# Kernel tuning notes

Hardware: AMD Instinct MI355X
Metric: run time of the kernel (lower is better)

Reference implementation:

```python
import jax, jax.numpy as jnp
import numpy as np


def conv2d(x, w, b, pad=0, groups=1):
    y = jax.lax.conv_general_dilated(
        x, w, (1, 1), [(pad, pad), (pad, pad)],
        dimension_numbers=('NCHW', 'OIHW', 'NCHW'), feature_group_count=groups)
    return y + b[None, :, None, None]


def layernorm(x, w, b, eps=1e-5):
    # per-pixel LayerNorm over channel dim (matches to_3d -> nn.LayerNorm(dim) -> to_4d)
    mu = x.mean(1, keepdims=True)
    var = ((x - mu) ** 2).mean(1, keepdims=True)
    return (x - mu) * jax.lax.rsqrt(var + eps) * w[None, :, None, None] + b[None, :, None, None]


def setup_inputs():
    key = jax.random.key(0)
    ks = jax.random.split(key, 16)
    B, C, H, W = 1, 64, 64, 64
    heads, dh = 8, 8
    inner = heads * dh          # 64
    hid_lc = 32                 # max(16, inner // 2)
    hid_f = 4 * C               # 256, ffn_expansion_factor = 4
    def s(k, shape, fan):
        return (jax.random.normal(k, shape, jnp.float32) / np.float32(np.sqrt(fan)))
    return {
        'x': jax.random.normal(ks[0], (B, C, H, W), jnp.float32),
        'luma': jax.random.uniform(ks[1], (B, 1, H, W), jnp.float32),
        'ln1_w': jnp.ones((C,), jnp.float32), 'ln1_b': jnp.zeros((C,), jnp.float32),
        'qkv_w': s(ks[2], (3 * inner, C, 1, 1), C), 'qkv_b': jnp.zeros((3 * inner,), jnp.float32),
        'proj_w': s(ks[3], (C, inner, 1, 1), inner), 'proj_b': jnp.zeros((C,), jnp.float32),
        'lc1_w': s(ks[4], (hid_lc, 1, 3, 3), 9), 'lc1_b': jnp.zeros((hid_lc,), jnp.float32),
        'lc2_w': s(ks[5], (hid_lc, hid_lc, 3, 3), 9 * hid_lc), 'lc2_b': jnp.zeros((hid_lc,), jnp.float32),
        'gam_w': s(ks[6], (inner, hid_lc, 1, 1), hid_lc), 'gam_b': jnp.zeros((inner,), jnp.float32),
        'bet_w': s(ks[7], (inner, hid_lc, 1, 1), hid_lc), 'bet_b': jnp.zeros((inner,), jnp.float32),
        'alpha': jnp.float32(0.1),
        'ln2_w': jnp.ones((C,), jnp.float32), 'ln2_b': jnp.zeros((C,), jnp.float32),
        'ffn1_w': s(ks[8], (hid_f, C, 1, 1), C), 'ffn1_b': jnp.zeros((hid_f,), jnp.float32),
        'dw_w': s(ks[9], (hid_f, 1, 3, 3), 9), 'dw_b': jnp.zeros((hid_f,), jnp.float32),
        'ffn2_w': s(ks[10], (C, hid_f, 1, 1), hid_f), 'ffn2_b': jnp.zeros((C,), jnp.float32),
    }


def reference(x, luma, ln1_w, ln1_b, qkv_w, qkv_b, proj_w, proj_b,
              lc1_w, lc1_b, lc2_w, lc2_b, gam_w, gam_b, bet_w, bet_b, alpha,
              ln2_w, ln2_b, ffn1_w, ffn1_b, dw_w, dw_b, ffn2_w, ffn2_b):
    B, C, H, W = x.shape
    heads = 8
    N = H * W
    # --- attention branch ---
    xn = layernorm(x, ln1_w, ln1_b)
    qkv = conv2d(xn, qkv_w, qkv_b)             # [B, 3*inner, H, W]
    inner = qkv.shape[1] // 3
    dh = inner // heads

    def to_bhnd(t):  # b (h d) x y -> b h (x y) d
        return t.reshape(B, heads, dh, N).transpose(0, 1, 3, 2)

    q, k, v = [to_bhnd(t) for t in jnp.split(qkv, 3, axis=1)]
    # luma conditioning
    h1 = jax.nn.relu(conv2d(luma, lc1_w, lc1_b, pad=1))
    h1 = jax.nn.relu(conv2d(h1, lc2_w, lc2_b, pad=1))
    g = to_bhnd(conv2d(h1, gam_w, gam_b))
    bt = to_bhnd(conv2d(h1, bet_w, bet_b))
    q = g * q + bt
    k = g * k + bt
    v = g * v + bt
    # additive luma bias on q (avg_pool2d 3x3, count_include_pad=True -> fixed /9)
    invL = 1.0 - luma
    invL = jax.lax.reduce_window(invL, 0.0, jax.lax.add, (1, 1, 3, 3), (1, 1, 1, 1),
                                 [(0, 0), (0, 0), (1, 1), (1, 1)]) / 9.0
    invL = invL.reshape(B, N)
    invL = invL - invL.mean(-1, keepdims=True)
    q = q + alpha * invL[:, None, :, None]
    scale = dh ** -0.5
    attn = jax.nn.softmax(jnp.einsum('bhid,bhjd->bhij', q, k) * scale, axis=-1)
    out = jnp.einsum('bhij,bhjd->bhid', attn, v)
    out = out.transpose(0, 1, 3, 2).reshape(B, inner, H, W)
    x = x + conv2d(out, proj_w, proj_b)
    # --- ConvFFN branch ---
    y = layernorm(x, ln2_w, ln2_b)
    y = conv2d(y, ffn1_w, ffn1_b)
    y = conv2d(y, dw_w, dw_b, pad=1, groups=y.shape[1])
    y = jax.nn.gelu(y, approximate=False)
    y = conv2d(y, ffn2_w, ffn2_b)
    return x + y
```

## Files before the change

kernel.cpp:

```cpp
#include <hip/hip_runtime.h>
#include <math.h>

#define NPIX 4096
#define IMG 64

typedef __attribute__((ext_vector_type(8))) short bf16x8;
typedef __attribute__((ext_vector_type(4))) float floatx4;
typedef __attribute__((ext_vector_type(4))) unsigned int uintx4;

__device__ __forceinline__ unsigned int split_pack(float x) {
  unsigned int u = __float_as_uint(x);
  unsigned int hif = u & 0xffff0000u;
  float lof = x - __uint_as_float(hif);
  return (u >> 16) | (__float_as_uint(lof) & 0xffff0000u);
}

__device__ __forceinline__ unsigned int hi_pair(float a, float b) {
  return (__float_as_uint(a) >> 16) | (__float_as_uint(b) & 0xffff0000u);
}

__global__ __launch_bounds__(256) void lc1_kernel(
    const float* __restrict__ luma, const float* __restrict__ w1,
    const float* __restrict__ b1, float* __restrict__ h1,
    float* __restrict__ pooled, float* __restrict__ bsums,
    unsigned short* __restrict__ cbuf) {
  __shared__ float red[256];
  int tile = blockIdx.x, ocg = blockIdx.y;
  int tid = threadIdx.x;
  if (tile == 0 && ocg == 0 && tid < 16) cbuf[tid] = (tid < 8) ? 0x3F80 : 0;
  int p = tile * 256 + tid;
  int py = p >> 6, px = p & 63;
  float v[9];
#pragma unroll
  for (int dy = 0; dy < 3; dy++)
#pragma unroll
    for (int dx = 0; dx < 3; dx++) {
      int y = py + dy - 1, x = px + dx - 1;
      v[dy * 3 + dx] =
          (y >= 0 && y < IMG && x >= 0 && x < IMG) ? luma[y * IMG + x] : 0.f;
    }
#pragma unroll
  for (int o = 0; o < 4; o++) {
    int oc = ocg * 4 + o;
    float s = b1[oc];
#pragma unroll
    for (int t = 0; t < 9; t++) s = fmaf(w1[oc * 9 + t], v[t], s);
    h1[oc * NPIX + p] = fmaxf(s, 0.f);
  }
  if (ocg == 0) {
    float sv = 0.f;
#pragma unroll
    for (int t = 0; t < 9; t++) sv += v[t];
    float cy = 3.f - (py == 0 ? 1.f : 0.f) - (py == 63 ? 1.f : 0.f);
    float cx = 3.f - (px == 0 ? 1.f : 0.f) - (px == 63 ? 1.f : 0.f);
    float pv = (cy * cx - sv) * (1.f / 9.f);
    pooled[p] = pv;
    red[tid] = pv;
    __syncthreads();
    for (int st = 128; st > 0; st >>= 1) {
      if (tid < st) red[tid] += red[tid + st];
      __syncthreads();
    }
    if (tid == 0) bsums[tile] = red[0];
  }
}

__global__ __launch_bounds__(256) void lc2_kernel(
    const float* __restrict__ h1, const float* __restrict__ w2,
    const float* __restrict__ b2, const float* __restrict__ x,
    float* __restrict__ h2, float* __restrict__ mu1, float* __restrict__ rs1) {
  __shared__ float tin[32][324];
  __shared__ float swt[4][32][9];
  int tile = blockIdx.x, ocg = blockIdx.y;
  int ty0 = (tile >> 2) * 16, tx0 = (tile & 3) * 16;
  int tid = threadIdx.x;
  for (int idx = tid; idx < 32 * 324; idx += 256) {
    int ic = idx / 324, pos = idx - ic * 324;
    int py = pos / 18, px = pos - py * 18;
    int gy = ty0 + py - 1, gx = tx0 + px - 1;
    tin[ic][pos] = (gy >= 0 && gy < IMG && gx >= 0 && gx < IMG)
                       ? h1[ic * NPIX + gy * IMG + gx]
                       : 0.f;
  }
  for (int idx = tid; idx < 4 * 32 * 9; idx += 256) {
    int o = idx / 288, r = idx - o * 288;
    swt[o][r / 9][r % 9] = w2[(ocg * 4 + o) * 288 + r];
  }
  __syncthreads();
  int ly = tid >> 4, lx = tid & 15;
  int p = (ty0 + ly) * IMG + tx0 + lx;
  float acc[4];
#pragma unroll
  for (int o = 0; o < 4; o++) acc[o] = b2[ocg * 4 + o];
  for (int ic = 0; ic < 32; ic++) {
    float v[9];
#pragma unroll
    for (int dy = 0; dy < 3; dy++)
#pragma unroll
      for (int dx = 0; dx < 3; dx++)
        v[dy * 3 + dx] = tin[ic][(ly + dy) * 18 + lx + dx];
#pragma unroll
    for (int o = 0; o < 4; o++)
#pragma unroll
      for (int t = 0; t < 9; t++) acc[o] = fmaf(swt[o][ic][t], v[t], acc[o]);
  }
#pragma unroll
  for (int o = 0; o < 4; o++)
    h2[(ocg * 4 + o) * NPIX + p] = fmaxf(acc[o], 0.f);
  if (ocg == 0) {
    float s = 0.f, q = 0.f;
#pragma unroll 8
    for (int cc = 0; cc < 64; cc++) {
      float xv = x[cc * NPIX + p];
      s += xv;
      q = fmaf(xv, xv, q);
    }
    float mu = s * (1.f / 64.f);
    mu1[p] = mu;
    rs1[p] = rsqrtf(q * (1.f / 64.f) - mu * mu + 1e-5f);
  }
}

__global__ __launch_bounds__(256) void ln_qkv_kernel(
    const float* __restrict__ X, const float* __restrict__ mu1,
    const float* __restrict__ rs1, const float* __restrict__ lnw,
    const float* __restrict__ lnb, const float* __restrict__ W,
    const float* __restrict__ bias, const float* __restrict__ gamW,
    const float* __restrict__ gamB, const float* __restrict__ betW,
    const float* __restrict__ betB, const float* __restrict__ h2,
    const float* __restrict__ pooled, const float* __restrict__ bsums,
    const float* __restrict__ alpha, unsigned short* __restrict__ qhl,
    unsigned short* __restrict__ khl, unsigned short* __restrict__ vthx,
    unsigned short* __restrict__ vtlx) {
  const float QSCALE = 0.35355339059327376f * 1.4426950408889634f;
  __shared__ float xs[64][64];
  __shared__ float wsh[64][64];
  __shared__ float h2s[32][64];
  __shared__ float wgs[32][64];
  __shared__ float wbs[32][64];
  __shared__ float mu[64];
  __shared__ float rs[64];
  int n0 = blockIdx.x * 64, part = blockIdx.y, m0 = part * 64;
  int tid = threadIdx.x;
  int c = tid >> 2, pg = (tid & 3) * 16;
  if (tid < 64) {
    mu[tid] = mu1[n0 + tid];
    rs[tid] = rs1[n0 + tid];
  }
  {
    const float4* src = (const float4*)&X[c * NPIX + n0 + pg];
    float4* dst = (float4*)&xs[c][pg];
    dst[0] = src[0]; dst[1] = src[1]; dst[2] = src[2]; dst[3] = src[3];
  }
  {
    int m = tid >> 2, kg = (tid & 3) * 16;
    const float4* wr = (const float4*)&W[(m0 + m) * 64 + kg];
    float4 w0 = wr[0], w1 = wr[1], w2 = wr[2], w3 = wr[3];
    float wv[16] = {w0.x, w0.y, w0.z, w0.w, w1.x, w1.y, w1.z, w1.w,
                    w2.x, w2.y, w2.z, w2.w, w3.x, w3.y, w3.z, w3.w};
#pragma unroll
    for (int j = 0; j < 16; j++) wsh[kg + j][m] = wv[j];
  }
  {
    int i0 = tid * 2;
    int k = i0 >> 4, nf = (i0 & 15) * 4;
    *(float4*)&h2s[k][nf] = *(const float4*)&h2[k * NPIX + n0 + nf];
    int i1 = i0 + 1;
    int k1 = i1 >> 4, nf1 = (i1 & 15) * 4;
    *(float4*)&h2s[k1][nf1] = *(const float4*)&h2[k1 * NPIX + n0 + nf1];
  }
  {
    int m = tid >> 2, kg = (tid & 3) * 8;
    const float4* g0 = (const float4*)&gamW[m * 32 + kg];
    float4 a = g0[0], b4 = g0[1];
    float gv[8] = {a.x, a.y, a.z, a.w, b4.x, b4.y, b4.z, b4.w};
#pragma unroll
    for (int j = 0; j < 8; j++) wgs[kg + j][m] = gv[j];
    const float4* bb0 = (const float4*)&betW[m * 32 + kg];
    float4 c4 = bb0[0], d4 = bb0[1];
    float bv[8] = {c4.x, c4.y, c4.z, c4.w, d4.x, d4.y, d4.z, d4.w};
#pragma unroll
    for (int j = 0; j < 8; j++) wbs[kg + j][m] = bv[j];
  }
  __syncthreads();
  {
    float wc = lnw[c], bc = lnb[c];
#pragma unroll
    for (int j = 0; j < 16; j++) {
      int p = pg + j;
      xs[c][p] = (xs[c][p] - mu[p]) * rs[p] * wc + bc;
    }
  }
  __syncthreads();
  int tx = tid & 15, ty = tid >> 4;
  float ga[4][4] = {}, ba[4][4] = {};
#pragma unroll 8
  for (int kk = 0; kk < 32; kk++) {
    float4 wg4 = *(const float4*)&wgs[kk][ty * 4];
    float4 wb4 = *(const float4*)&wbs[kk][ty * 4];
    float4 h24 = *(const float4*)&h2s[kk][tx * 4];
    float gv[4] = {wg4.x, wg4.y, wg4.z, wg4.w};
    float bv[4] = {wb4.x, wb4.y, wb4.z, wb4.w};
    float hv[4] = {h24.x, h24.y, h24.z, h24.w};
#pragma unroll
    for (int im = 0; im < 4; im++)
#pragma unroll
      for (int in = 0; in < 4; in++) {
        ga[im][in] = fmaf(gv[im], hv[in], ga[im][in]);
        ba[im][in] = fmaf(bv[im], hv[in], ba[im][in]);
      }
  }
#pragma unroll
  for (int im = 0; im < 4; im++) {
    int cc = ty * 4 + im;
    float gb = gamB[cc], bb2 = betB[cc];
#pragma unroll
    for (int in = 0; in < 4; in++) {
      ga[im][in] += gb;
      ba[im][in] += bb2;
    }
  }
  float acc[4][4] = {};
#pragma unroll 8
  for (int kk = 0; kk < 64; kk++) {
    float4 a = *(const float4*)&wsh[kk][ty * 4];
    float4 b4 = *(const float4*)&xs[kk][tx * 4];
    float av[4] = {a.x, a.y, a.z, a.w};
    float bv[4] = {b4.x, b4.y, b4.z, b4.w};
#pragma unroll
    for (int im = 0; im < 4; im++)
#pragma unroll
      for (int in = 0; in < 4; in++)
        acc[im][in] = fmaf(av[im], bv[in], acc[im][in]);
  }
  float val[4][4];
#pragma unroll
  for (int im = 0; im < 4; im++) {
    int cc = ty * 4 + im;
    float bv = bias[m0 + cc];
#pragma unroll
    for (int in = 0; in < 4; in++)
      val[im][in] = fmaf(ga[im][in], acc[im][in] + bv, ba[im][in]);
  }
  if (part == 0) {
    float msum = 0.f;
#pragma unroll
    for (int t = 0; t < 16; t++) msum += bsums[t];
    float mean = msum * (1.f / 4096.f);
    float a0 = alpha[0];
    const float4 pv = *(const float4*)&pooled[n0 + tx * 4];
    float iv[4] = {a0 * (pv.x - mean), a0 * (pv.y - mean),
                   a0 * (pv.z - mean), a0 * (pv.w - mean)};
#pragma unroll
    for (int im = 0; im < 4; im++)
#pragma unroll
      for (int in = 0; in < 4; in++)
        val[im][in] = (val[im][in] + iv[in]) * QSCALE;
  }
  if (part < 2) {
    unsigned short* dst = (part == 0) ? qhl : khl;
    int h = ty >> 1, d0 = (ty & 1) * 4;
#pragma unroll
    for (int in = 0; in < 4; in++) {
      int n = n0 + tx * 4 + in;
      unsigned int pk[4];
#pragma unroll
      for (int im = 0; im < 4; im++) pk[im] = split_pack(val[im][in]);
      short4 hi, lo;
      hi.x = (short)(pk[0] & 0xffffu); hi.y = (short)(pk[1] & 0xffffu);
      hi.z = (short)(pk[2] & 0xffffu); hi.w = (short)(pk[3] & 0xffffu);
      lo.x = (short)(pk[0] >> 16); lo.y = (short)(pk[1] >> 16);
      lo.z = (short)(pk[2] >> 16); lo.w = (short)(pk[3] >> 16);
      unsigned short* base = dst + ((size_t)(h * NPIX + n) << 4) + d0;
      *(short4*)base = hi;
      *(short4*)(base + 8) = lo;
    }
  } else {
    int nq = n0 + tx * 4;
    int off0 = (nq >> 5) * 32 + ((nq >> 4) & 1) * 4 + ((nq >> 2) & 3) * 8;
#pragma unroll
    for (int im = 0; im < 4; im++) {
      int cc = ty * 4 + im;
      unsigned int pk[4];
#pragma unroll
      for (int in = 0; in < 4; in++) pk[in] = split_pack(val[im][in]);
      short4 hi, lo;
      hi.x = (short)(pk[0] & 0xffffu); hi.y = (short)(pk[1] & 0xffffu);
      hi.z = (short)(pk[2] & 0xffffu); hi.w = (short)(pk[3] & 0xffffu);
      lo.x = (short)(pk[0] >> 16); lo.y = (short)(pk[1] >> 16);
      lo.z = (short)(pk[2] >> 16); lo.w = (short)(pk[3] >> 16);
      *(short4*)(vthx + (size_t)cc * NPIX + off0) = hi;
      *(short4*)(vtlx + (size_t)cc * NPIX + off0) = lo;
    }
  }
}

__global__ __launch_bounds__(256, 6) void attn_kernel(
    const unsigned short* __restrict__ qhl,
    const unsigned short* __restrict__ khl,
    const unsigned short* __restrict__ vthx,
    const unsigned short* __restrict__ vtlx,
    const unsigned short* __restrict__ cbuf, float* __restrict__ pacc,
    float* __restrict__ pl) {
  int tid = threadIdx.x;
  int wave = tid >> 6, lane = tid & 63;
  int g = lane >> 4, c = lane & 15;
  int h = blockIdx.y, jp = blockIdx.z;
  int i0 = blockIdx.x * 128 + wave * 32;
  int jbase = jp * 512;
  const bf16x8 qB0 = *(const bf16x8*)(qhl + ((size_t)(h * NPIX + i0 + c) << 4) +
                                      ((g & 1) << 3));
  const bf16x8 qB1 = *(const bf16x8*)(
      qhl + ((size_t)(h * NPIX + i0 + 16 + c) << 4) + ((g & 1) << 3));
  const unsigned short* kp =
      khl + ((size_t)(h * NPIX + jbase + c) << 4) + ((g >> 1) << 3);
  const unsigned short* vhp;
  const unsigned short* vlp;
  int vstep;
  if (c < 8) {
    vhp = vthx + (size_t)(h * 8 + c) * NPIX + jbase + (g << 3);
    vlp = vtlx + (size_t)(h * 8 + c) * NPIX + jbase + (g << 3);
    vstep = 32;
  } else {
    vhp = (c == 8) ? cbuf : (cbuf + 8);
    vlp = cbuf + 8;
    vstep = 0;
  }
  floatx4 zero4 = {0.f, 0.f, 0.f, 0.f};
  floatx4 aH0 = zero4, aM0 = zero4, aH1 = zero4, aM1 = zero4;
#pragma unroll 2
  for (int jt = 0; jt < 16; ++jt) {
    bf16x8 ka0 = *(const bf16x8*)kp;
    bf16x8 ka1 = *(const bf16x8*)(kp + 256);
    bf16x8 avh = *(const bf16x8*)vhp;
    bf16x8 avl = *(const bf16x8*)vlp;
    kp += 512;
    vhp += vstep;
    vlp += vstep;
    floatx4 s00 =
        __builtin_amdgcn_mfma_f32_16x16x32_bf16(ka0, qB0, zero4, 0, 0, 0);
    floatx4 s01 =
        __builtin_amdgcn_mfma_f32_16x16x32_bf16(ka1, qB0, zero4, 0, 0, 0);
    floatx4 s10 =
        __builtin_amdgcn_mfma_f32_16x16x32_bf16(ka0, qB1, zero4, 0, 0, 0);
    floatx4 s11 =
        __builtin_amdgcn_mfma_f32_16x16x32_bf16(ka1, qB1, zero4, 0, 0, 0);
    {
      float p0 = __builtin_amdgcn_exp2f(fminf(s00[0], 80.f));
      float p1 = __builtin_amdgcn_exp2f(fminf(s00[1], 80.f));
      float p2 = __builtin_amdgcn_exp2f(fminf(s00[2], 80.f));
      float p3 = __builtin_amdgcn_exp2f(fminf(s00[3], 80.f));
      float p4 = __builtin_amdgcn_exp2f(fminf(s01[0], 80.f));
      float p5 = __builtin_amdgcn_exp2f(fminf(s01[1], 80.f));
      float p6 = __builtin_amdgcn_exp2f(fminf(s01[2], 80.f));
      float p7 = __builtin_amdgcn_exp2f(fminf(s01[3], 80.f));
      uintx4 bh;
      bh.x = hi_pair(p0, p1);
      bh.y = hi_pair(p2, p3);
      bh.z = hi_pair(p4, p5);
      bh.w = hi_pair(p6, p7);
      bf16x8 pbh = __builtin_bit_cast(bf16x8, bh);
      aH0 = __builtin_amdgcn_mfma_f32_16x16x32_bf16(avh, pbh, aH0, 0, 0, 0);
      aM0 = __builtin_amdgcn_mfma_f32_16x16x32_bf16(avl, pbh, aM0, 0, 0, 0);
    }
    {
      float p0 = __builtin_amdgcn_exp2f(fminf(s10[0], 80.f));
      float p1 = __builtin_amdgcn_exp2f(fminf(s10[1], 80.f));
      float p2 = __builtin_amdgcn_exp2f(fminf(s10[2], 80.f));
      float p3 = __builtin_amdgcn_exp2f(fminf(s10[3], 80.f));
      float p4 = __builtin_amdgcn_exp2f(fminf(s11[0], 80.f));
      float p5 = __builtin_amdgcn_exp2f(fminf(s11[1], 80.f));
      float p6 = __builtin_amdgcn_exp2f(fminf(s11[2], 80.f));
      float p7 = __builtin_amdgcn_exp2f(fminf(s11[3], 80.f));
      uintx4 bh;
      bh.x = hi_pair(p0, p1);
      bh.y = hi_pair(p2, p3);
      bh.z = hi_pair(p4, p5);
      bh.w = hi_pair(p6, p7);
      bf16x8 pbh = __builtin_bit_cast(bf16x8, bh);
      aH1 = __builtin_amdgcn_mfma_f32_16x16x32_bf16(avh, pbh, aH1, 0, 0, 0);
      aM1 = __builtin_amdgcn_mfma_f32_16x16x32_bf16(avl, pbh, aM1, 0, 0, 0);
    }
  }
  floatx4 o0 = aH0 + aM0;
  floatx4 o1 = aH1 + aM1;
  if (g < 2) {
    size_t b0 = (size_t)((jp * 8 + h) * NPIX + i0 + c);
    *(float4*)&pacc[b0 * 8 + g * 4] = make_float4(o0[0], o0[1], o0[2], o0[3]);
    size_t b1 = b0 + 16;
    *(float4*)&pacc[b1 * 8 + g * 4] = make_float4(o1[0], o1[1], o1[2], o1[3]);
  } else if (g == 2) {
    pl[(size_t)((jp * 8 + h) * NPIX + i0 + c)] = o0[0];
    pl[(size_t)((jp * 8 + h) * NPIX + i0 + 16 + c)] = o1[0];
  }
}

__global__ __launch_bounds__(256) void proj_ffn1_kernel(
    const float* __restrict__ pacc, const float* __restrict__ pl,
    const float* __restrict__ Wp, const float* __restrict__ bp,
    const float* __restrict__ x, const float* __restrict__ ln2w,
    const float* __restrict__ ln2b, const float* __restrict__ W1,
    const float* __restrict__ b1f, float* __restrict__ x1,
    float* __restrict__ f1) {
  __shared__ float at[64][33];
  __shared__ float wsh[64][64];
  __shared__ float xsl[64][33];
  __shared__ float ps[8][33];
  __shared__ float pq[8][33];
  __shared__ float mus[32];
  __shared__ float rss[32];
  int n0 = blockIdx.x * 32;
  int ch = blockIdx.y;
  int tid = threadIdx.x;
  {
    int mm = tid >> 2, kg = (tid & 3) * 16;
    const float4* wr = (const float4*)&Wp[mm * 64 + kg];
    float4 w0 = wr[0], w1 = wr[1], w2 = wr[2], w3 = wr[3];
    float wv[16] = {w0.x, w0.y, w0.z, w0.w, w1.x, w1.y, w1.z, w1.w,
                    w2.x, w2.y, w2.z, w2.w, w3.x, w3.y, w3.z, w3.w};
#pragma unroll
    for (int j = 0; j < 16; j++) wsh[kg + j][mm] = wv[j];
  }
  {
    int hh = tid >> 5, nn = tid & 31;
    int i = n0 + nn;
    float L = 0.f, o[8] = {};
#pragma unroll
    for (int p = 0; p < 8; p++) {
      size_t base = (size_t)((p * 8 + hh) * NPIX + i);
      L += pl[base];
      const float4 a0 = *(const float4*)&pacc[base * 8];
      const float4 a1 = *(const float4*)&pacc[base * 8 + 4];
      o[0] += a0.x; o[1] += a0.y; o[2] += a0.z; o[3] += a0.w;
      o[4] += a1.x; o[5] += a1.y; o[6] += a1.z; o[7] += a1.w;
    }
    float inv = 1.f / L;
#pragma unroll
    for (int d = 0; d < 8; d++) at[hh * 8 + d][nn] = o[d] * inv;
  }
  __syncthreads();
  int ty = tid >> 5, tx = tid & 31;
  float acc[8] = {};
#pragma unroll 8
  for (int k = 0; k < 64; k++) {
    float b = at[k][tx];
    float4 a0 = *(const float4*)&wsh[k][ty * 8];
    float4 a1 = *(const float4*)&wsh[k][ty * 8 + 4];
    acc[0] = fmaf(a0.x, b, acc[0]);
    acc[1] = fmaf(a0.y, b, acc[1]);
    acc[2] = fmaf(a0.z, b, acc[2]);
    acc[3] = fmaf(a0.w, b, acc[3]);
    acc[4] = fmaf(a1.x, b, acc[4]);
    acc[5] = fmaf(a1.y, b, acc[5]);
    acc[6] = fmaf(a1.z, b, acc[6]);
    acc[7] = fmaf(a1.w, b, acc[7]);
  }
  float v[8], sn = 0.f, qn = 0.f;
#pragma unroll
  for (int im = 0; im < 8; im++) {
    int row = ty * 8 + im;
    float vv = acc[im] + bp[row] + x[row * NPIX + n0 + tx];
    v[im] = vv;
    sn += vv;
    qn = fmaf(vv, vv, qn);
  }
  if (ch == 0) {
#pragma unroll
    for (int im = 0; im < 8; im++)
      x1[(ty * 8 + im) * NPIX + n0 + tx] = v[im];
  }
  ps[ty][tx] = sn;
  pq[ty][tx] = qn;
  __syncthreads();
  if (tid < 32) {
    float s = 0.f, q = 0.f;
#pragma unroll
    for (int t = 0; t < 8; t++) {
      s += ps[t][tid];
      q += pq[t][tid];
    }
    float mu = s * (1.f / 64.f);
    mus[tid] = mu;
    rss[tid] = rsqrtf(q * (1.f / 64.f) - mu * mu + 1e-5f);
  }
  __syncthreads();
  {
    float muv = mus[tx], rsv = rss[tx];
#pragma unroll
    for (int im = 0; im < 8; im++) {
      int row = ty * 8 + im;
      xsl[row][tx] = (v[im] - muv) * rsv * ln2w[row] + ln2b[row];
    }
  }
  {
    int mm = tid >> 2, kg = (tid & 3) * 16;
    const float4* wr = (const float4*)&W1[(ch * 64 + mm) * 64 + kg];
    float4 w0 = wr[0], w1 = wr[1], w2 = wr[2], w3 = wr[3];
    float wv[16] = {w0.x, w0.y, w0.z, w0.w, w1.x, w1.y, w1.z, w1.w,
                    w2.x, w2.y, w2.z, w2.w, w3.x, w3.y, w3.z, w3.w};
#pragma unroll
    for (int j = 0; j < 16; j++) wsh[kg + j][mm] = wv[j];
  }
  __syncthreads();
  float a2[8] = {};
#pragma unroll 8
  for (int k = 0; k < 64; k++) {
    float b = xsl[k][tx];
    float4 a0 = *(const float4*)&wsh[k][ty * 8];
    float4 a1 = *(const float4*)&wsh[k][ty * 8 + 4];
    a2[0] = fmaf(a0.x, b, a2[0]);
    a2[1] = fmaf(a0.y, b, a2[1]);
    a2[2] = fmaf(a0.z, b, a2[2]);
    a2[3] = fmaf(a0.w, b, a2[3]);
    a2[4] = fmaf(a1.x, b, a2[4]);
    a2[5] = fmaf(a1.y, b, a2[5]);
    a2[6] = fmaf(a1.z, b, a2[6]);
    a2[7] = fmaf(a1.w, b, a2[7]);
  }
#pragma unroll
  for (int im = 0; im < 8; im++) {
    int row = ch * 64 + ty * 8 + im;
    f1[row * NPIX + n0 + tx] = a2[im] + b1f[row];
  }
}

__global__ __launch_bounds__(256) void dw_gelu_kernel(
    const float* __restrict__ f1, const float* __restrict__ w,
    const float* __restrict__ b, float* __restrict__ f2) {
  int t = blockIdx.x * 256 + threadIdx.x;
  int c = t >> 10, pq = t & 1023;
  int py = pq >> 4, px0 = (pq & 15) << 2;
  const float* base = f1 + c * NPIX;
  float wv[9];
#pragma unroll
  for (int i = 0; i < 9; i++) wv[i] = w[c * 9 + i];
  float bc = b[c];
  float a[4] = {bc, bc, bc, bc};
#pragma unroll
  for (int dy = 0; dy < 3; dy++) {
    int y = py + dy - 1;
    if (y < 0 || y > 63) continue;
    const float* row = base + y * IMG + px0;
    float4 mid = *(const float4*)row;
    float left = (px0 > 0) ? row[-1] : 0.f;
    float right = (px0 < 60) ? row[4] : 0.f;
    float win[6] = {left, mid.x, mid.y, mid.z, mid.w, right};
#pragma unroll
    for (int o = 0; o < 4; o++)
#pragma unroll
      for (int dx = 0; dx < 3; dx++)
        a[o] = fmaf(wv[dy * 3 + dx], win[o + dx], a[o]);
  }
  float4 o4;
  float* op = &o4.x;
#pragma unroll
  for (int o = 0; o < 4; o++)
    op[o] = 0.5f * a[o] * (1.f + erff(a[o] * 0.70710678118654752f));
  *(float4*)&f2[c * NPIX + py * IMG + px0] = o4;
}

__global__ __launch_bounds__(256) void gemm16_kernel(
    const float* __restrict__ W, const float* __restrict__ X,
    const float* __restrict__ bias, const float* __restrict__ resid,
    float* __restrict__ C, int K) {
  __shared__ float xs[32][64];
  __shared__ float wsh[32][16];
  int n0 = blockIdx.x * 64, m0 = blockIdx.y * 16;
  int tid = threadIdx.x;
  int m = tid >> 4, ng = tid & 15;
  float acc[4] = {};
  for (int k0 = 0; k0 < K; k0 += 32) {
    {
      int i0 = tid * 2;
      int k = i0 >> 4, nf = (i0 & 15) * 4;
      *(float4*)&xs[k][nf] = *(const float4*)&X[(k0 + k) * NPIX + n0 + nf];
      int i1 = i0 + 1;
      int k1 = i1 >> 4, nf1 = (i1 & 15) * 4;
      *(float4*)&xs[k1][nf1] = *(const float4*)&X[(k0 + k1) * NPIX + n0 + nf1];
    }
#pragma unroll
    for (int e = tid; e < 512; e += 256) {
      int mm = e >> 5, kk = e & 31;
      wsh[kk][mm] = W[(m0 + mm) * K + k0 + kk];
    }
    __syncthreads();
#pragma unroll 8
    for (int kk = 0; kk < 32; kk++) {
      float a = wsh[kk][m];
      float4 b4 = *(const float4*)&xs[kk][ng * 4];
      acc[0] = fmaf(a, b4.x, acc[0]);
      acc[1] = fmaf(a, b4.y, acc[1]);
      acc[2] = fmaf(a, b4.z, acc[2]);
      acc[3] = fmaf(a, b4.w, acc[3]);
    }
    __syncthreads();
  }
  int row = m0 + m;
  float bv = bias[row];
  float4 o = make_float4(acc[0] + bv, acc[1] + bv, acc[2] + bv, acc[3] + bv);
  const float4 r4 = *(const float4*)&resid[row * NPIX + n0 + ng * 4];
  o.x += r4.x; o.y += r4.y; o.z += r4.z; o.w += r4.w;
  *(float4*)&C[row * NPIX + n0 + ng * 4] = o;
}

extern "C" void kernel_launch(void* const* d_in, const int* in_sizes, int n_in,
                              void* d_out, int out_size, void* d_ws,
                              size_t ws_size, hipStream_t stream) {
  const float* x      = (const float*)d_in[0];
  const float* luma   = (const float*)d_in[1];
  const float* ln1_w  = (const float*)d_in[2];
  const float* ln1_b  = (const float*)d_in[3];
  const float* qkv_w  = (const float*)d_in[4];
  const float* qkv_b  = (const float*)d_in[5];
  const float* proj_w = (const float*)d_in[6];
  const float* proj_b = (const float*)d_in[7];
  const float* lc1_w  = (const float*)d_in[8];
  const float* lc1_b  = (const float*)d_in[9];
  const float* lc2_w  = (const float*)d_in[10];
  const float* lc2_b  = (const float*)d_in[11];
  const float* gam_w  = (const float*)d_in[12];
  const float* gam_b  = (const float*)d_in[13];
  const float* bet_w  = (const float*)d_in[14];
  const float* bet_b  = (const float*)d_in[15];
  const float* alpha  = (const float*)d_in[16];
  const float* ln2_w  = (const float*)d_in[17];
  const float* ln2_b  = (const float*)d_in[18];
  const float* ffn1_w = (const float*)d_in[19];
  const float* ffn1_b = (const float*)d_in[20];
  const float* dw_w   = (const float*)d_in[21];
  const float* dw_b   = (const float*)d_in[22];
  const float* ffn2_w = (const float*)d_in[23];
  const float* ffn2_b = (const float*)d_in[24];
  float* out = (float*)d_out;

  float* w = (float*)d_ws;
  float* pooled = w + 0;
  float* bsums  = w + 4096;
  unsigned short* cbuf = (unsigned short*)(w + 4160);
  float* mu1 = w + 4224;
  float* rs1 = w + 8320;
  unsigned short* qhl  = (unsigned short*)(w + 12416);
  unsigned short* khl  = (unsigned short*)(w + 274560);
  unsigned short* vthx = (unsigned short*)(w + 536704);
  unsigned short* vtlx = (unsigned short*)(w + 667776);
  float* pacc = w + 798848;
  float* pl   = w + 2896000;
  float* x1   = w + 3158144;
  float* f1   = w + 3420288;
  float* f2   = w + 4468864;
  float* h2   = w + 5517440;
  float* h1   = w + 5648512;

  lc1_kernel<<<dim3(16, 8), 256, 0, stream>>>(luma, lc1_w, lc1_b, h1, pooled,
                                              bsums, cbuf);
  lc2_kernel<<<dim3(16, 8), 256, 0, stream>>>(h1, lc2_w, lc2_b, x, h2, mu1,
                                              rs1);
  ln_qkv_kernel<<<dim3(64, 3), 256, 0, stream>>>(
      x, mu1, rs1, ln1_w, ln1_b, qkv_w, qkv_b, gam_w, gam_b, bet_w, bet_b, h2,
      pooled, bsums, alpha, qhl, khl, vthx, vtlx);
  attn_kernel<<<dim3(32, 8, 8), 256, 0, stream>>>(qhl, khl, vthx, vtlx, cbuf,
                                                  pacc, pl);
  proj_ffn1_kernel<<<dim3(128, 4), 256, 0, stream>>>(
      pacc, pl, proj_w, proj_b, x, ln2_w, ln2_b, ffn1_w, ffn1_b, x1, f1);
  dw_gelu_kernel<<<1024, 256, 0, stream>>>(f1, dw_w, dw_b, f2);
  gemm16_kernel<<<dim3(64, 4), 256, 0, stream>>>(ffn2_w, f2, ffn2_b, x1, out,
                                                 256);
}
```

Before: 205.9 us.

## Halve attention key-split count and load full K in single-pass FFN2 kernel

The attention kernel now splits keys into 4 partitions of 1024 instead of 8 of 512. That halves the partial accumulator traffic and the reduction work in the proj kernel, but leaves fewer blocks in flight, so the occupancy hint drops from 6 to 4. The FFN2 GEMM is rewritten to stage all 256 K values of X and W in shared memory at once, using 32-column tiles and doubling the grid, which removes the per-chunk sync loop. This raises shared memory per block to about 48KB, which may limit occupancy.

```diff
diff --git a/kernel.cpp b/kernel.cpp
--- a/kernel.cpp
+++ b/kernel.cpp
@@ -295,7 +295,7 @@
   }
 }
 
-__global__ __launch_bounds__(256, 6) void attn_kernel(
+__global__ __launch_bounds__(256, 4) void attn_kernel(
     const unsigned short* __restrict__ qhl,
     const unsigned short* __restrict__ khl,
     const unsigned short* __restrict__ vthx,
@@ -307,7 +307,7 @@
   int g = lane >> 4, c = lane & 15;
   int h = blockIdx.y, jp = blockIdx.z;
   int i0 = blockIdx.x * 128 + wave * 32;
-  int jbase = jp * 512;
+  int jbase = jp * 1024;
   const bf16x8 qB0 = *(const bf16x8*)(qhl + ((size_t)(h * NPIX + i0 + c) << 4) +
                                       ((g & 1) << 3));
   const bf16x8 qB1 = *(const bf16x8*)(
@@ -329,7 +329,7 @@
   floatx4 zero4 = {0.f, 0.f, 0.f, 0.f};
   floatx4 aH0 = zero4, aM0 = zero4, aH1 = zero4, aM1 = zero4;
 #pragma unroll 2
-  for (int jt = 0; jt < 16; ++jt) {
+  for (int jt = 0; jt < 32; ++jt) {
     bf16x8 ka0 = *(const bf16x8*)kp;
     bf16x8 ka1 = *(const bf16x8*)(kp + 256);
     bf16x8 avh = *(const bf16x8*)vhp;
@@ -426,7 +426,7 @@
     int i = n0 + nn;
     float L = 0.f, o[8] = {};
 #pragma unroll
-    for (int p = 0; p < 8; p++) {
+    for (int p = 0; p < 4; p++) {
       size_t base = (size_t)((p * 8 + hh) * NPIX + i);
       L += pl[base];
       const float4 a0 = *(const float4*)&pacc[base * 8];
@@ -559,48 +559,39 @@
   *(float4*)&f2[c * NPIX + py * IMG + px0] = o4;
 }
 
-__global__ __launch_bounds__(256) void gemm16_kernel(
+__global__ __launch_bounds__(256) void ffn2_kernel(
     const float* __restrict__ W, const float* __restrict__ X,
     const float* __restrict__ bias, const float* __restrict__ resid,
-    float* __restrict__ C, int K) {
-  __shared__ float xs[32][64];
-  __shared__ float wsh[32][16];
-  int n0 = blockIdx.x * 64, m0 = blockIdx.y * 16;
+    float* __restrict__ C) {
+  __shared__ float xs[256][32];
+  __shared__ float wsh[256][16];
+  int n0 = blockIdx.x * 32, m0 = blockIdx.y * 16;
   int tid = threadIdx.x;
-  int m = tid >> 4, ng = tid & 15;
-  float acc[4] = {};
-  for (int k0 = 0; k0 < K; k0 += 32) {
-    {
-      int i0 = tid * 2;
-      int k = i0 >> 4, nf = (i0 & 15) * 4;
-      *(float4*)&xs[k][nf] = *(const float4*)&X[(k0 + k) * NPIX + n0 + nf];
-      int i1 = i0 + 1;
-      int k1 = i1 >> 4, nf1 = (i1 & 15) * 4;
-      *(float4*)&xs[k1][nf1] = *(const float4*)&X[(k0 + k1) * NPIX + n0 + nf1];
-    }
-#pragma unroll
-    for (int e = tid; e < 512; e += 256) {
-      int mm = e >> 5, kk = e & 31;
-      wsh[kk][mm] = W[(m0 + mm) * K + k0 + kk];
-    }
-    __syncthreads();
+#pragma unroll
+  for (int e = tid; e < 2048; e += 256) {
+    int k = e >> 3, nf = (e & 7) * 4;
+    *(float4*)&xs[k][nf] = *(const float4*)&X[k * NPIX + n0 + nf];
+  }
+#pragma unroll
+  for (int e = tid; e < 4096; e += 256) {
+    int mm = e >> 8, kk = e & 255;
+    wsh[kk][mm] = W[(m0 + mm) * 256 + kk];
+  }
+  __syncthreads();
+  int m = tid >> 4, np = (tid & 15) * 2;
+  float acc0 = 0.f, acc1 = 0.f;
 #pragma unroll 8
-    for (int kk = 0; kk < 32; kk++) {
-      float a = wsh[kk][m];
-      float4 b4 = *(const float4*)&xs[kk][ng * 4];
-      acc[0] = fmaf(a, b4.x, acc[0]);
-      acc[1] = fmaf(a, b4.y, acc[1]);
-      acc[2] = fmaf(a, b4.z, acc[2]);
-      acc[3] = fmaf(a, b4.w, acc[3]);
-    }
-    __syncthreads();
+  for (int kk = 0; kk < 256; kk++) {
+    float a = wsh[kk][m];
+    float2 b2 = *(const float2*)&xs[kk][np];
+    acc0 = fmaf(a, b2.x, acc0);
+    acc1 = fmaf(a, b2.y, acc1);
   }
   int row = m0 + m;
   float bv = bias[row];
-  float4 o = make_float4(acc[0] + bv, acc[1] + bv, acc[2] + bv, acc[3] + bv);
-  const float4 r4 = *(const float4*)&resid[row * NPIX + n0 + ng * 4];
-  o.x += r4.x; o.y += r4.y; o.z += r4.z; o.w += r4.w;
-  *(float4*)&C[row * NPIX + n0 + ng * 4] = o;
+  const float2 r2 = *(const float2*)&resid[row * NPIX + n0 + np];
+  float2 o = make_float2(acc0 + bv + r2.x, acc1 + bv + r2.y);
+  *(float2*)&C[row * NPIX + n0 + np] = o;
 }
 
 extern "C" void kernel_launch(void* const* d_in, const int* in_sizes, int n_in,
@@ -644,12 +635,12 @@
   unsigned short* vthx = (unsigned short*)(w + 536704);
   unsigned short* vtlx = (unsigned short*)(w + 667776);
   float* pacc = w + 798848;
-  float* pl   = w + 2896000;
-  float* x1   = w + 3158144;
-  float* f1   = w + 3420288;
-  float* f2   = w + 4468864;
-  float* h2   = w + 5517440;
-  float* h1   = w + 5648512;
+  float* pl   = w + 1847424;
+  float* x1   = w + 1978496;
+  float* f1   = w + 2240640;
+  float* f2   = w + 3289216;
+  float* h2   = w + 4337792;
+  float* h1   = w + 4468864;
 
   lc1_kernel<<<dim3(16, 8), 256, 0, stream>>>(luma, lc1_w, lc1_b, h1, pooled,
                                               bsums, cbuf);
@@ -658,11 +649,10 @@
   ln_qkv_kernel<<<dim3(64, 3), 256, 0, stream>>>(
       x, mu1, rs1, ln1_w, ln1_b, qkv_w, qkv_b, gam_w, gam_b, bet_w, bet_b, h2,
       pooled, bsums, alpha, qhl, khl, vthx, vtlx);
-  attn_kernel<<<dim3(32, 8, 8), 256, 0, stream>>>(qhl, khl, vthx, vtlx, cbuf,
+  attn_kernel<<<dim3(32, 8, 4), 256, 0, stream>>>(qhl, khl, vthx, vtlx, cbuf,
                                                   pacc, pl);
   proj_ffn1_kernel<<<dim3(128, 4), 256, 0, stream>>>(
       pacc, pl, proj_w, proj_b, x, ln2_w, ln2_b, ffn1_w, ffn1_b, x1, f1);
   dw_gelu_kernel<<<1024, 256, 0, stream>>>(f1, dw_w, dw_b, f2);
-  gemm16_kernel<<<dim3(64, 4), 256, 0, stream>>>(ffn2_w, f2, ffn2_b, x1, out,
-                                                 256);
-}
+  ffn2_kernel<<<dim3(128, 4), 256, 0, stream>>>(ffn2_w, f2, ffn2_b, x1, out);
+}
```

New measurement: 202.6 us. Within noise of the previous version (-1.6%).
